# Kernel optimization log

Hardware: AMD Instinct MI355X
Metric: run time of the kernel (lower is better)

## Reference

```python
import jax, jax.numpy as jnp
import numpy as np

DIM = 512

def setup_inputs() -> dict:
    key = jax.random.key(0)
    ks = jax.random.split(key, 8)
    B, T, S, D = 4, 128, 512, DIM
    scale = 1.0 / np.sqrt(D)
    return {
        "inp": jax.random.normal(ks[0], (B, T, D), jnp.float32),
        "context": jax.random.normal(ks[1], (B, S, D), jnp.float32),
        # linear_query: Linear(D, D, bias=True)
        "Wq": jax.random.normal(ks[2], (D, D), jnp.float32) * scale,
        "bq": jax.random.normal(ks[3], (D,), jnp.float32) * scale,
        # linear_context: Linear(D, D, bias=False)
        "Wc": jax.random.normal(ks[4], (D, D), jnp.float32) * scale,
        # v: Linear(D, 1, bias=False)
        "v": jax.random.normal(ks[5], (D,), jnp.float32) * scale,
        # linear_out: Linear(2D, D, bias=True)
        "Wout": jax.random.normal(ks[6], (D, 2 * D), jnp.float32) * scale,
        "bout": jax.random.normal(ks[7], (D,), jnp.float32) * scale,
    }

def reference(inp, context, Wq, bq, Wc, v, Wout, bout):
    # inp: (B,T,D) target queries; context: (B,S,D) source states
    wq = jnp.einsum('btd,ed->bte', inp, Wq) + bq          # (B,T,D)
    uh = jnp.einsum('bsd,ed->bse', context, Wc)            # (B,S,D)
    # additive (Bahdanau) score: v^T tanh(Wq q_t + Wc h_s)
    wquh = jnp.tanh(wq[:, :, None, :] + uh[:, None, :, :])  # (B,T,S,D)
    align = jnp.einsum('btsd,d->bts', wquh, v)             # (B,T,S)
    align_vectors = jax.nn.softmax(align, axis=-1)          # softmax over src_len
    c = jnp.einsum('bts,bsd->btd', align_vectors, context)  # context vector
    concat_c = jnp.concatenate([c, inp], axis=-1)           # (B,T,2D)
    attn_h = jnp.einsum('btf,ef->bte', concat_c, Wout) + bout  # (B,T,D)
    return attn_h, align_vectors
```

## Files before the change

### kernel.cpp

```cpp
#include <hip/hip_runtime.h>
#include <hip/hip_bf16.h>
#include <math.h>


typedef __attribute__((ext_vector_type(8))) short short8;
typedef __attribute__((ext_vector_type(4))) float f32x4;
typedef unsigned short ushort_t;

static __device__ __forceinline__ unsigned short f2bf(float x) {
    union { __hip_bfloat16 h; unsigned short u; } c;
    c.h = __float2bfloat16(x);
    return c.u;
}
static __device__ __forceinline__ int bf2x(float lo, float hi) {
    return (int)(((unsigned)f2bf(hi) << 16) | (unsigned)f2bf(lo));
}

template<bool BF>
static __device__ __forceinline__ void load16(const void* base, size_t elemoff,
                                              int4& r0, int4& r1) {
    if (BF) {
        const int4* p = (const int4*)((const ushort_t*)base + elemoff);
        r0 = p[0]; r1 = p[1];
    } else {
        const float4* p = (const float4*)((const float*)base + elemoff);
        float4 a = p[0], b = p[1], c = p[2], d = p[3];
        r0.x = bf2x(a.x, a.y); r0.y = bf2x(a.z, a.w);
        r0.z = bf2x(b.x, b.y); r0.w = bf2x(b.z, b.w);
        r1.x = bf2x(c.x, c.y); r1.y = bf2x(c.z, c.w);
        r1.z = bf2x(d.x, d.y); r1.w = bf2x(d.z, d.w);
    }
}

template<bool A_BF, bool W_BF, int EPI>
static __device__ __forceinline__ void gemm_body(
    ushort_t* As, ushort_t* Ws,
    const void* A, const void* W, const float* bias, const float* partial,
    void* Cv, int K, int lda, int ldw, int ldc, int bm, int bn)
{
    const int tid = threadIdx.x;
    const int wave = tid >> 6, lane = tid & 63;
    const int mh = (wave & 1) * 32, nh = (wave >> 1) * 32;
    const int quad = lane >> 4, l16 = lane & 15;
    const int srow = tid >> 2, schunk = tid & 3;

    const size_t aoff = (size_t)(bm + srow) * lda + schunk * 16;
    const size_t woff = (size_t)(bn + srow) * ldw + schunk * 16;
    int4* AsW = (int4*)&As[srow * 72 + schunk * 16];
    int4* WsW = (int4*)&Ws[srow * 72 + schunk * 16];

    f32x4 acc00 = {0.f, 0.f, 0.f, 0.f}, acc01 = acc00, acc10 = acc00, acc11 = acc00;

    int4 a0r, a1r, w0r, w1r;
    load16<A_BF>(A, aoff, a0r, a1r);
    load16<W_BF>(W, woff, w0r, w1r);

    for (int k0 = 0; k0 < K; k0 += 64) {
        AsW[0] = a0r; AsW[1] = a1r;
        WsW[0] = w0r; WsW[1] = w1r;
        __syncthreads();
        if (k0 + 64 < K) {
            load16<A_BF>(A, aoff + k0 + 64, a0r, a1r);
            load16<W_BF>(W, woff + k0 + 64, w0r, w1r);
        }
        #pragma unroll
        for (int kk = 0; kk < 64; kk += 32) {
            short8 a0 = *(const short8*)&As[(mh + l16) * 72 + kk + quad * 8];
            short8 a1 = *(const short8*)&As[(mh + 16 + l16) * 72 + kk + quad * 8];
            short8 b0 = *(const short8*)&Ws[(nh + l16) * 72 + kk + quad * 8];
            short8 b1 = *(const short8*)&Ws[(nh + 16 + l16) * 72 + kk + quad * 8];
            acc00 = __builtin_amdgcn_mfma_f32_16x16x32_bf16(a0, b0, acc00, 0, 0, 0);
            acc01 = __builtin_amdgcn_mfma_f32_16x16x32_bf16(a0, b1, acc01, 0, 0, 0);
            acc10 = __builtin_amdgcn_mfma_f32_16x16x32_bf16(a1, b0, acc10, 0, 0, 0);
            acc11 = __builtin_amdgcn_mfma_f32_16x16x32_bf16(a1, b1, acc11, 0, 0, 0);
        }
        __syncthreads();
    }

    const int col0 = bn + nh + l16;
    const int col1 = col0 + 16;
    float bias0 = bias ? bias[col0] : 0.f;
    float bias1 = bias ? bias[col1] : 0.f;

    f32x4 accs[2][2] = {{acc00, acc01}, {acc10, acc11}};
    #pragma unroll
    for (int mt = 0; mt < 2; ++mt) {
        #pragma unroll
        for (int r = 0; r < 4; ++r) {
            int row = bm + mh + mt * 16 + quad * 4 + r;
            size_t rowoff = (size_t)row * ldc;
            float v0 = accs[mt][0][r] + bias0;
            float v1 = accs[mt][1][r] + bias1;
            if (EPI == 1) { v0 = __expf(2.f * v0); v1 = __expf(2.f * v1); }
            if (EPI == 3) { v0 += partial[rowoff + col0]; v1 += partial[rowoff + col1]; }
            if (EPI == 2) {
                ushort_t* C = (ushort_t*)Cv;
                C[rowoff + col0] = f2bf(v0);
                C[rowoff + col1] = f2bf(v1);
            } else {
                float* C = (float*)Cv;
                C[rowoff + col0] = v0;
                C[rowoff + col1] = v1;
            }
        }
    }
}

__global__ __launch_bounds__(256) void fused_front(
    const float* __restrict__ inp, const float* __restrict__ ctx,
    const float* __restrict__ Wq, const float* __restrict__ bq,
    const float* __restrict__ Wc, const float* __restrict__ Wout,
    const float* __restrict__ bout,
    float* __restrict__ Ew, float* __restrict__ Eu, float* __restrict__ Y0,
    ushort_t* __restrict__ GT)
{
    __shared__ ushort_t As[64 * 72];
    __shared__ ushort_t Ws[64 * 72];
    const int bid = blockIdx.x;

    if (bid < 64) {
        gemm_body<false, false, 1>(As, Ws, inp, Wq, bq, nullptr, Ew,
                                   512, 512, 512, 512, (bid & 7) * 64, (bid >> 3) * 64);
    } else if (bid < 320) {
        int i = bid - 64;
        gemm_body<false, false, 1>(As, Ws, ctx, Wc, nullptr, nullptr, Eu,
                                   512, 512, 512, 512, (i & 31) * 64, (i >> 5) * 64);
    } else if (bid < 576) {
        int i = bid - 320;
        int b = i >> 6, j = i & 63;
        gemm_body<false, false, 2>(As, Ws, Wout, ctx + (size_t)b * 262144, nullptr,
                                   nullptr, GT + (size_t)b * 262144,
                                   512, 1024, 512, 512, (j & 7) * 64, (j >> 3) * 64);
    } else {
        int i = bid - 576;
        gemm_body<false, false, 0>(As, Ws, inp, Wout + 512, bout, nullptr, Y0,
                                   512, 512, 1024, 512, (i & 7) * 64, (i >> 3) * 64);
    }
}

__global__ __launch_bounds__(256) void align_kernel(
    const float* __restrict__ Ew, const float* __restrict__ Eu,
    const float* __restrict__ v, float* __restrict__ out)
{
    const int lane = threadIdx.x & 63, wave = threadIdx.x >> 6;
    const int b = blockIdx.z;
    const int t0 = blockIdx.y * 16 + wave * 4;
    const int s0 = blockIdx.x * 8;

    const float* wp = Ew + (((size_t)(b * 128 + t0)) << 9);
    const float* up = Eu + (((size_t)(b * 512 + s0)) << 9);

    float acc[4][8];
    #pragma unroll
    for (int i = 0; i < 4; ++i)
        #pragma unroll
        for (int j = 0; j < 8; ++j) acc[i][j] = 0.f;
    float vsum = 0.f;

    for (int k0 = 0; k0 < 512; k0 += 64) {
        float vk = v[k0 + lane];
        vsum += vk;
        float w0 = wp[k0 + lane];
        float w1 = wp[512 + k0 + lane];
        float w2 = wp[1024 + k0 + lane];
        float w3 = wp[1536 + k0 + lane];
        #pragma unroll
        for (int j = 0; j < 8; ++j) {
            float u = up[((size_t)j << 9) + k0 + lane];
            float d0 = fmaf(w0, u, 1.f);
            float d1 = fmaf(w1, u, 1.f);
            float d2 = fmaf(w2, u, 1.f);
            float d3 = fmaf(w3, u, 1.f);
            float r0 = __builtin_amdgcn_rcpf(d0);
            float r1 = __builtin_amdgcn_rcpf(d1);
            float r2 = __builtin_amdgcn_rcpf(d2);
            float r3 = __builtin_amdgcn_rcpf(d3);
            acc[0][j] = fmaf(vk, r0, acc[0][j]);
            acc[1][j] = fmaf(vk, r1, acc[1][j]);
            acc[2][j] = fmaf(vk, r2, acc[2][j]);
            acc[3][j] = fmaf(vk, r3, acc[3][j]);
        }
    }

    float V = vsum;
    #pragma unroll
    for (int off = 32; off; off >>= 1) V += __shfl_xor(V, off, 64);

    float r0 = 0.f, r1 = 0.f, r2 = 0.f, r3 = 0.f;
    #pragma unroll
    for (int j = 0; j < 8; ++j) {
        float a0 = acc[0][j], a1 = acc[1][j], a2 = acc[2][j], a3 = acc[3][j];
        #pragma unroll
        for (int off = 32; off; off >>= 1) {
            a0 += __shfl_xor(a0, off, 64);
            a1 += __shfl_xor(a1, off, 64);
            a2 += __shfl_xor(a2, off, 64);
            a3 += __shfl_xor(a3, off, 64);
        }
        if (lane == j) {
            r0 = fmaf(-2.f, a0, V);
            r1 = fmaf(-2.f, a1, V);
            r2 = fmaf(-2.f, a2, V);
            r3 = fmaf(-2.f, a3, V);
        }
    }
    if (lane < 8) {
        size_t o = (((size_t)(b * 128 + t0)) << 9) + s0 + lane;
        out[o] = r0;
        out[o + 512] = r1;
        out[o + 1024] = r2;
        out[o + 1536] = r3;
    }
}

__global__ __launch_bounds__(256) void softmax_512(
    const float* __restrict__ Sraw, float* __restrict__ alignv,
    ushort_t* __restrict__ pbf)
{
    const int row = blockIdx.x;
    const float* p = Sraw + ((size_t)row << 9);
    float* a = alignv + ((size_t)row << 9);
    ushort_t* q = pbf + ((size_t)row << 9);
    const int tid = threadIdx.x;
    float x0 = p[tid];
    float x1 = p[tid + 256];

    float m = fmaxf(x0, x1);
    #pragma unroll
    for (int off = 32; off > 0; off >>= 1)
        m = fmaxf(m, __shfl_xor(m, off, 64));
    __shared__ float redm[4];
    __shared__ float reds[4];
    const int wave = tid >> 6;
    if ((tid & 63) == 0) redm[wave] = m;
    __syncthreads();
    m = fmaxf(fmaxf(redm[0], redm[1]), fmaxf(redm[2], redm[3]));

    float e0 = __expf(x0 - m);
    float e1 = __expf(x1 - m);
    float s = e0 + e1;
    #pragma unroll
    for (int off = 32; off > 0; off >>= 1)
        s += __shfl_xor(s, off, 64);
    if ((tid & 63) == 0) reds[wave] = s;
    __syncthreads();
    s = reds[0] + reds[1] + reds[2] + reds[3];
    float r = 1.0f / s;
    float p0 = e0 * r, p1 = e1 * r;
    a[tid] = p0;
    a[tid + 256] = p1;
    q[tid] = f2bf(p0);
    q[tid + 256] = f2bf(p1);
}

__global__ __launch_bounds__(256) void gemm_att(
    const ushort_t* __restrict__ P, const ushort_t* __restrict__ GT,
    const float* __restrict__ Y0, float* __restrict__ attn)
{
    __shared__ ushort_t As[64 * 72];
    __shared__ ushort_t Ws[64 * 72];
    const int b = blockIdx.z;
    gemm_body<true, true, 3>(As, Ws,
                             P + (size_t)b * 65536, GT + (size_t)b * 262144,
                             nullptr, Y0 + (size_t)b * 65536,
                             attn + (size_t)b * 65536,
                             512, 512, 512, 512, blockIdx.x * 64, blockIdx.y * 64);
}

extern "C" void kernel_launch(void* const* d_in, const int* in_sizes, int n_in,
                              void* d_out, int out_size, void* d_ws, size_t ws_size,
                              hipStream_t stream)
{
    const float* inp  = (const float*)d_in[0];
    const float* ctx  = (const float*)d_in[1];
    const float* Wq   = (const float*)d_in[2];
    const float* bq   = (const float*)d_in[3];
    const float* Wc   = (const float*)d_in[4];
    const float* v    = (const float*)d_in[5];
    const float* Wout = (const float*)d_in[6];
    const float* bout = (const float*)d_in[7];

    float* out    = (float*)d_out;
    float* attn   = out;
    float* alignv = out + 262144;

    float* ws = (float*)d_ws;
    float* Ew   = ws;
    float* Eu   = ws + 262144;
    float* Y0   = ws + 1310720;
    float* Sraw = ws + 1572864;
    ushort_t* GT   = (ushort_t*)(ws + 1835008);
    ushort_t* P_bf = (ushort_t*)(ws + 2359296);

    fused_front<<<dim3(640), 256, 0, stream>>>(inp, ctx, Wq, bq, Wc, Wout, bout,
                                               Ew, Eu, Y0, GT);
    align_kernel<<<dim3(64, 8, 4), 256, 0, stream>>>(Ew, Eu, v, Sraw);
    softmax_512<<<dim3(512), 256, 0, stream>>>(Sraw, alignv, P_bf);
    gemm_att<<<dim3(2, 8, 4), 256, 0, stream>>>(P_bf, GT, Y0, attn);
}
```

Measured before the change: 121.4 us.

## Store exp-transformed query/context projections in bf16 and enlarge align register tile

The Wq and Wc projection epilogues now write exp(2x) as bf16 instead of fp32, halving the Ew/Eu traffic that the align kernel streams. The align kernel reads packed bf16 pairs and unpacks them with shifts and masks. Each wave now covers 8 query rows instead of 4, which doubles reuse of every loaded context element and halves the grid. This costs precision in the tanh-based scores, since bf16 rounding of exp(2x) feeds 1/(1+ab), and the larger accumulator array raises register pressure.

```diff
diff --git a/kernel.cpp b/kernel.cpp
--- a/kernel.cpp
+++ b/kernel.cpp
@@ -14,6 +14,12 @@
 }
 static __device__ __forceinline__ int bf2x(float lo, float hi) {
     return (int)(((unsigned)f2bf(hi) << 16) | (unsigned)f2bf(lo));
+}
+static __device__ __forceinline__ float bfu_lo(unsigned u) {
+    union { unsigned u; float f; } c; c.u = u << 16; return c.f;
+}
+static __device__ __forceinline__ float bfu_hi(unsigned u) {
+    union { unsigned u; float f; } c; c.u = u & 0xffff0000u; return c.f;
 }
 
 template<bool BF>
@@ -91,9 +97,9 @@
             size_t rowoff = (size_t)row * ldc;
             float v0 = accs[mt][0][r] + bias0;
             float v1 = accs[mt][1][r] + bias1;
-            if (EPI == 1) { v0 = __expf(2.f * v0); v1 = __expf(2.f * v1); }
+            if (EPI == 1 || EPI == 4) { v0 = __expf(2.f * v0); v1 = __expf(2.f * v1); }
             if (EPI == 3) { v0 += partial[rowoff + col0]; v1 += partial[rowoff + col1]; }
-            if (EPI == 2) {
+            if (EPI == 2 || EPI == 4) {
                 ushort_t* C = (ushort_t*)Cv;
                 C[rowoff + col0] = f2bf(v0);
                 C[rowoff + col1] = f2bf(v1);
@@ -111,19 +117,19 @@
     const float* __restrict__ Wq, const float* __restrict__ bq,
     const float* __restrict__ Wc, const float* __restrict__ Wout,
     const float* __restrict__ bout,
-    float* __restrict__ Ew, float* __restrict__ Eu, float* __restrict__ Y0,
-    ushort_t* __restrict__ GT)
+    ushort_t* __restrict__ Ew, ushort_t* __restrict__ Eu,
+    float* __restrict__ Y0, ushort_t* __restrict__ GT)
 {
     __shared__ ushort_t As[64 * 72];
     __shared__ ushort_t Ws[64 * 72];
     const int bid = blockIdx.x;
 
     if (bid < 64) {
-        gemm_body<false, false, 1>(As, Ws, inp, Wq, bq, nullptr, Ew,
+        gemm_body<false, false, 4>(As, Ws, inp, Wq, bq, nullptr, Ew,
                                    512, 512, 512, 512, (bid & 7) * 64, (bid >> 3) * 64);
     } else if (bid < 320) {
         int i = bid - 64;
-        gemm_body<false, false, 1>(As, Ws, ctx, Wc, nullptr, nullptr, Eu,
+        gemm_body<false, false, 4>(As, Ws, ctx, Wc, nullptr, nullptr, Eu,
                                    512, 512, 512, 512, (i & 31) * 64, (i >> 5) * 64);
     } else if (bid < 576) {
         int i = bid - 320;
@@ -139,46 +145,46 @@
 }
 
 __global__ __launch_bounds__(256) void align_kernel(
-    const float* __restrict__ Ew, const float* __restrict__ Eu,
+    const ushort_t* __restrict__ Ew, const ushort_t* __restrict__ Eu,
     const float* __restrict__ v, float* __restrict__ out)
 {
     const int lane = threadIdx.x & 63, wave = threadIdx.x >> 6;
     const int b = blockIdx.z;
-    const int t0 = blockIdx.y * 16 + wave * 4;
+    const int t0 = blockIdx.y * 32 + wave * 8;
     const int s0 = blockIdx.x * 8;
 
-    const float* wp = Ew + (((size_t)(b * 128 + t0)) << 9);
-    const float* up = Eu + (((size_t)(b * 512 + s0)) << 9);
-
-    float acc[4][8];
-    #pragma unroll
-    for (int i = 0; i < 4; ++i)
+    const unsigned* wp = (const unsigned*)(Ew + (((size_t)(b * 128 + t0)) << 9));
+    const unsigned* up = (const unsigned*)(Eu + (((size_t)(b * 512 + s0)) << 9));
+
+    float acc[8][8];
+    #pragma unroll
+    for (int i = 0; i < 8; ++i)
         #pragma unroll
         for (int j = 0; j < 8; ++j) acc[i][j] = 0.f;
     float vsum = 0.f;
 
-    for (int k0 = 0; k0 < 512; k0 += 64) {
-        float vk = v[k0 + lane];
-        vsum += vk;
-        float w0 = wp[k0 + lane];
-        float w1 = wp[512 + k0 + lane];
-        float w2 = wp[1024 + k0 + lane];
-        float w3 = wp[1536 + k0 + lane];
+    for (int c0 = 0; c0 < 256; c0 += 64) {
+        float2 vk = *(const float2*)&v[(c0 + lane) * 2];
+        vsum += vk.x + vk.y;
+        float wlo[8], whi[8];
+        #pragma unroll
+        for (int tt = 0; tt < 8; ++tt) {
+            unsigned wu = wp[tt * 256 + c0 + lane];
+            wlo[tt] = bfu_lo(wu);
+            whi[tt] = bfu_hi(wu);
+        }
         #pragma unroll
         for (int j = 0; j < 8; ++j) {
-            float u = up[((size_t)j << 9) + k0 + lane];
-            float d0 = fmaf(w0, u, 1.f);
-            float d1 = fmaf(w1, u, 1.f);
-            float d2 = fmaf(w2, u, 1.f);
-            float d3 = fmaf(w3, u, 1.f);
-            float r0 = __builtin_amdgcn_rcpf(d0);
-            float r1 = __builtin_amdgcn_rcpf(d1);
-            float r2 = __builtin_amdgcn_rcpf(d2);
-            float r3 = __builtin_amdgcn_rcpf(d3);
-            acc[0][j] = fmaf(vk, r0, acc[0][j]);
-            acc[1][j] = fmaf(vk, r1, acc[1][j]);
-            acc[2][j] = fmaf(vk, r2, acc[2][j]);
-            acc[3][j] = fmaf(vk, r3, acc[3][j]);
+            unsigned uu = up[j * 256 + c0 + lane];
+            float ulo = bfu_lo(uu), uhi = bfu_hi(uu);
+            #pragma unroll
+            for (int tt = 0; tt < 8; ++tt) {
+                float dl = fmaf(wlo[tt], ulo, 1.f);
+                float dh = fmaf(whi[tt], uhi, 1.f);
+                float rl = __builtin_amdgcn_rcpf(dl);
+                float rh = __builtin_amdgcn_rcpf(dh);
+                acc[tt][j] = fmaf(vk.x, rl, fmaf(vk.y, rh, acc[tt][j]));
+            }
         }
     }
 
@@ -186,30 +192,40 @@
     #pragma unroll
     for (int off = 32; off; off >>= 1) V += __shfl_xor(V, off, 64);
 
-    float r0 = 0.f, r1 = 0.f, r2 = 0.f, r3 = 0.f;
+    float res[8];
+    #pragma unroll
+    for (int tt = 0; tt < 8; ++tt) res[tt] = 0.f;
     #pragma unroll
     for (int j = 0; j < 8; ++j) {
         float a0 = acc[0][j], a1 = acc[1][j], a2 = acc[2][j], a3 = acc[3][j];
+        float a4 = acc[4][j], a5 = acc[5][j], a6 = acc[6][j], a7 = acc[7][j];
         #pragma unroll
         for (int off = 32; off; off >>= 1) {
             a0 += __shfl_xor(a0, off, 64);
             a1 += __shfl_xor(a1, off, 64);
             a2 += __shfl_xor(a2, off, 64);
             a3 += __shfl_xor(a3, off, 64);
+            a4 += __shfl_xor(a4, off, 64);
+            a5 += __shfl_xor(a5, off, 64);
+            a6 += __shfl_xor(a6, off, 64);
+            a7 += __shfl_xor(a7, off, 64);
         }
         if (lane == j) {
-            r0 = fmaf(-2.f, a0, V);
-            r1 = fmaf(-2.f, a1, V);
-            r2 = fmaf(-2.f, a2, V);
-            r3 = fmaf(-2.f, a3, V);
+            res[0] = fmaf(-2.f, a0, V);
+            res[1] = fmaf(-2.f, a1, V);
+            res[2] = fmaf(-2.f, a2, V);
+            res[3] = fmaf(-2.f, a3, V);
+            res[4] = fmaf(-2.f, a4, V);
+            res[5] = fmaf(-2.f, a5, V);
+            res[6] = fmaf(-2.f, a6, V);
+            res[7] = fmaf(-2.f, a7, V);
         }
     }
     if (lane < 8) {
         size_t o = (((size_t)(b * 128 + t0)) << 9) + s0 + lane;
-        out[o] = r0;
-        out[o + 512] = r1;
-        out[o + 1024] = r2;
-        out[o + 1536] = r3;
+        #pragma unroll
+        for (int tt = 0; tt < 8; ++tt)
+            out[o + (size_t)tt * 512] = res[tt];
     }
 }
 
@@ -285,16 +301,16 @@
     float* alignv = out + 262144;
 
     float* ws = (float*)d_ws;
-    float* Ew   = ws;
-    float* Eu   = ws + 262144;
-    float* Y0   = ws + 1310720;
-    float* Sraw = ws + 1572864;
-    ushort_t* GT   = (ushort_t*)(ws + 1835008);
-    ushort_t* P_bf = (ushort_t*)(ws + 2359296);
+    ushort_t* Ew   = (ushort_t*)ws;
+    ushort_t* Eu   = (ushort_t*)(ws + 131072);
+    float* Y0      = ws + 655360;
+    float* Sraw    = ws + 917504;
+    ushort_t* GT   = (ushort_t*)(ws + 1179648);
+    ushort_t* P_bf = (ushort_t*)(ws + 1703936);
 
     fused_front<<<dim3(640), 256, 0, stream>>>(inp, ctx, Wq, bq, Wc, Wout, bout,
                                                Ew, Eu, Y0, GT);
-    align_kernel<<<dim3(64, 8, 4), 256, 0, stream>>>(Ew, Eu, v, Sraw);
+    align_kernel<<<dim3(64, 4, 4), 256, 0, stream>>>(Ew, Eu, v, Sraw);
     softmax_512<<<dim3(512), 256, 0, stream>>>(Sraw, alignv, P_bf);
     gemm_att<<<dim3(2, 8, 4), 256, 0, stream>>>(P_bf, GT, Y0, attn);
 }
```

After: 121.7 us. Within noise of the previous version (+0.2%).
